# Optimization experiments

Measured on AMD Instinct MI355X. Metric: run time of the kernel, lower is better.

## Reference

```python
import jax, jax.numpy as jnp
import numpy as np

N = 10000          # nodes
E = 160000         # random edges (self-loops added in reference, as PyG does)
HEADS = 32
DIMS = [4, 128, 512, 1028]
NEG_SLOPE_ATT = 0.2    # GATv2Conv default negative_slope
NEG_SLOPE_ACT = 0.01   # torch.nn.LeakyReLU default


def setup_inputs() -> dict:
    key = jax.random.key(0)
    ks = jax.random.split(key, 32)
    inp = {}
    inp["x"] = jax.random.normal(ks[0], (N, DIMS[0]), dtype=jnp.float32)
    inp["edge_index"] = jax.random.randint(ks[1], (2, E), 0, N, dtype=jnp.int32)
    k = 2
    for l in range(3):
        fi, fo = DIMS[l], DIMS[l + 1]
        s_in = 1.0 / np.sqrt(fi)
        s_att = 1.0 / np.sqrt(fo)
        inp[f"W{l+1}l"] = (jax.random.normal(ks[k], (fi, HEADS * fo)) * s_in).astype(jnp.float32); k += 1
        inp[f"b{l+1}l"] = jnp.zeros((HEADS * fo,), jnp.float32)
        inp[f"W{l+1}r"] = (jax.random.normal(ks[k], (fi, HEADS * fo)) * s_in).astype(jnp.float32); k += 1
        inp[f"b{l+1}r"] = jnp.zeros((HEADS * fo,), jnp.float32)
        inp[f"att{l+1}"] = (jax.random.normal(ks[k], (HEADS, fo)) * s_att).astype(jnp.float32); k += 1
        inp[f"bias{l+1}"] = jnp.zeros((fo,), jnp.float32)
    return inp


def gatv2_layer(x, src, dst, Wl, bl, Wr, br, att, bias):
    # x: [N, fi]; src/dst: [E'] (self-loops included); att: [H, C]
    H, C = att.shape
    n = x.shape[0]
    xl = (x @ Wl + bl).reshape(n, H, C)  # source transform
    xr = (x @ Wr + br).reshape(n, H, C)  # target transform

    def per_head(args):
        xlh, xrh, ah = args  # [N,C], [N,C], [C]
        s = jax.nn.leaky_relu(xlh[src] + xrh[dst], NEG_SLOPE_ATT)  # [E',C]
        e = s @ ah  # [E'] attention logits
        m = jax.ops.segment_max(e, dst, num_segments=n)
        p = jnp.exp(e - m[dst])
        den = jax.ops.segment_sum(p, dst, num_segments=n)
        alpha = p / den[dst]  # edge-softmax per destination
        return jax.ops.segment_sum(alpha[:, None] * xlh[src], dst, num_segments=n)  # [N,C]

    # iterate heads sequentially to keep peak memory at O(E*C), not O(E*H*C)
    out = jax.lax.map(per_head, (jnp.moveaxis(xl, 1, 0), jnp.moveaxis(xr, 1, 0), att))  # [H,N,C]
    return out.mean(axis=0) + bias  # concat=False -> head mean


def reference(x, edge_index, W1l, b1l, W1r, b1r, att1, bias1,
              W2l, b2l, W2r, b2r, att2, bias2,
              W3l, b3l, W3r, b3r, att3, bias3):
    n = x.shape[0]
    loop = jnp.arange(n, dtype=edge_index.dtype)
    src = jnp.concatenate([edge_index[0], loop])
    dst = jnp.concatenate([edge_index[1], loop])
    h = gatv2_layer(x, src, dst, W1l, b1l, W1r, b1r, att1, bias1)
    h = jax.nn.leaky_relu(h, NEG_SLOPE_ACT)
    h = gatv2_layer(h, src, dst, W2l, b2l, W2r, b2r, att2, bias2)
    h = jax.nn.leaky_relu(h, NEG_SLOPE_ACT)
    h = gatv2_layer(h, src, dst, W3l, b3l, W3r, b3r, att3, bias3)
    return h
```

## Files before the change

kernel.cpp:

```cpp
#include <hip/hip_runtime.h>
#include <cstddef>
#include <cstdint>


#define HEADS 32
#define SLOPE_ATT 0.2f
#define SLOPE_ACT 0.01f

typedef __bf16 bf16_t;
typedef __bf16 bf16x8 __attribute__((ext_vector_type(8)));
typedef float f32x16 __attribute__((ext_vector_type(16)));

#define GLDS16(gp, lp)                                                        \
  __builtin_amdgcn_global_load_lds(                                           \
      (const __attribute__((address_space(1))) void*)(gp),                    \
      (__attribute__((address_space(3))) void*)(lp), 16, 0, 0)


__global__ __launch_bounds__(256) void init_counts_kernel(int* counts, int n) {
  int i = blockIdx.x * 256 + threadIdx.x;
  if (i < n) counts[i] = 1;
}

__global__ __launch_bounds__(256) void count_kernel(const int* __restrict__ dst, int* counts, int E) {
  int e = blockIdx.x * 256 + threadIdx.x;
  if (e < E) atomicAdd(&counts[dst[e]], 1);
}

__global__ __launch_bounds__(1024) void scan_kernel(const int* __restrict__ counts,
                                                    int* __restrict__ row_ptr,
                                                    int* __restrict__ cursor, int n) {
  __shared__ int sums[1024];
  int t = threadIdx.x;
// ... 40 lines not shown
                                                       bf16_t* __restrict__ hi,
                                                       bf16_t* __restrict__ lo,
                                                       int M, int Mpad, int K) {
  int t = blockIdx.x * 256 + threadIdx.x;
  int kchunks = K >> 3;
  int total = Mpad * kchunks;
  if (t >= total) return;
  int kc = t % kchunks;
  int m = t / kchunks;
  int mt = m >> 7, ml = m & 127;
  size_t o = ((size_t)(mt * kchunks + kc)) * 1024 + (size_t)ml * 8;
  float v[8];
  if (m < M) {
    float4 a = *(const float4*)(X + (size_t)m * K + kc * 8);
    float4 b = *(const float4*)(X + (size_t)m * K + kc * 8 + 4);
    v[0] = a.x; v[1] = a.y; v[2] = a.z; v[3] = a.w;
    v[4] = b.x; v[5] = b.y; v[6] = b.z; v[7] = b.w;
  } else {
#pragma unroll
    for (int i = 0; i < 8; i++) v[i] = 0.f;
  }
  union { bf16_t h[8]; float4 f; } uh, ul;
#pragma unroll
  for (int i = 0; i < 8; i++) {
    bf16_t h = (bf16_t)v[i];
    uh.h[i] = h;
    ul.h[i] = (bf16_t)(v[i] - (float)h);
  }
  *(float4*)(hi + o) = uh.f;
  *(float4*)(lo + o) = ul.f;
}


__global__ __launch_bounds__(256) void pack_w_group_kernel(const float* __restrict__ Wl,
                                                           const float* __restrict__ Wr,
                                                           bf16_t* __restrict__ hL, bf16_t* __restrict__ lL,
                                                           bf16_t* __restrict__ hR, bf16_t* __restrict__ lR,
                                                           int K, int C, int Npad, int ldW,
                                                           int h0, int G) {
  int side = blockIdx.y;
  const float* W = side ? Wr : Wl;
  bf16_t* Hi = side ? hR : hL;
  bf16_t* Lo = side ? lR : lL;
  int kchunks = K >> 3;
  int perhead = Npad * kchunks;
  int t = blockIdx.x * 256 + threadIdx.x;
  if (t >= G * perhead) return;
  int g = t / perhead, rem = t % perhead;
  int n = rem % Npad, kc = rem / Npad;
  int nt = n >> 7, nl = n & 127;
  size_t o = (size_t)g * Npad * K + ((size_t)(nt * kchunks + kc)) * 1024 + (size_t)nl * 8;
  int col0 = (h0 + g) * C;
  union { bf16_t hh[8]; float4 f; } uh, ul;
#pragma unroll
  for (int kk = 0; kk < 8; kk++) {
    int k = kc * 8 + kk;
    float v = (n < C) ? W[(size_t)k * ldW + col0 + n] : 0.f;
    bf16_t hv = (bf16_t)v;
    uh.hh[kk] = hv;
    ul.hh[kk] = (bf16_t)(v - (float)hv);
  }
  *(float4*)(Hi + o) = uh.f;
  *(float4*)(Lo + o) = ul.f;
}


__global__ __launch_bounds__(256) void gemm_mfma_v6(const bf16_t* __restrict__ Xh,
                                                    const bf16_t* __restrict__ Xl,
                                                    const bf16_t* __restrict__ BhL,
                                                    const bf16_t* __restrict__ BlL,
                                                    const bf16_t* __restrict__ BhR,
                                                    const bf16_t* __restrict__ BlR,
                                                    size_t bHeadStride,
                                                    const float* __restrict__ bl,
                                                    const float* __restrict__ br,
                                                    float* __restrict__ outL,
                                                    float* __restrict__ outR,
                                                    size_t outHeadStride,
                                                    int M, int K, int C, int h0) {
  int gx = gridDim.x, gy = gridDim.y, gz = gridDim.z;
  int nwg = gx * gy * gz;
  int p = blockIdx.x + gx * (blockIdx.y + gy * blockIdx.z);
  int q = nwg >> 3, r = nwg & 7;
  int xcd = p & 7, slot = p >> 3;
  int lid = (xcd < r ? xcd * (q + 1) : r * (q + 1) + (xcd - r) * q) + slot;
  const int NY = 8;
  int xzsz = gx * gz;
  int fullr = gy / NY;
  int lidf = fullr * NY * xzsz;
  int rectbase, ny, rem;
  if (lid < lidf) {
    int rect = lid / (NY * xzsz);
    rem = lid - rect * (NY * xzsz);
    rectbase = rect * NY;
    ny = NY;
  } else {
    rem = lid - lidf;
    rectbase = fullr * NY;
    ny = gy - rectbase;
  }
  int xz = rem / ny;
  int yl = rem - xz * ny;
  int bx = xz % gx;
  int bz = xz / gx;
  int by = rectbase + yl;

  int g = bz >> 1, side = bz & 1;
  const bf16_t* Bh = (side ? BhR : BhL) + (size_t)g * bHeadStride;
  const bf16_t* Bl = (side ? BlR : BlL) + (size_t)g * bHeadStride;
  const float* bias = side ? br : bl;
  float* out = (side ? outR : outL) + (size_t)g * outHeadStride;
  int col0 = (h0 + g) * C;

  __shared__ __align__(16) bf16_t AsH[4 * 128 * 8];
  __shared__ __align__(16) bf16_t AsL[4 * 128 * 8];
  __shared__ __align__(16) bf16_t BsH[4 * 128 * 8];
  __shared__ __align__(16) bf16_t BsL[4 * 128 * 8];

  int tid = threadIdx.x;
  int wave = tid >> 6, lane = tid & 63;
  int l31 = lane & 31, lhalf = lane >> 5;
  int mt = by;
  int ntb = bx * 128;
  int m0 = mt * 128;
  int kchunks = K >> 3;

  const bf16_t* Ah = Xh + (size_t)mt * K * 128;
  const bf16_t* Al = Xl + (size_t)mt * K * 128;
  const bf16_t* Bhp = Bh + (size_t)bx * kchunks * 1024;
  const bf16_t* Blp = Bl + (size_t)bx * kchunks * 1024;

  auto* asH3 = (__attribute__((address_space(3))) bf16_t*)AsH;
  auto* asL3 = (__attribute__((address_space(3))) bf16_t*)AsL;
  auto* bsH3 = (__attribute__((address_space(3))) bf16_t*)BsH;
  auto* bsL3 = (__attribute__((address_space(3))) bf16_t*)BsL;

  f32x16 acc[4];
#pragma unroll
  for (int i = 0; i < 4; i++)
#pragma unroll
    for (int rr = 0; rr < 16; rr++) acc[i][rr] = 0.f;

  for (int k0 = 0; k0 < K; k0 += 32) {
    int kc0 = k0 >> 3;
#pragma unroll
    for (int rr = 0; rr < 2; rr++) {
      int idx = tid + 256 * rr;
      size_t off = ((size_t)(kc0 + (idx >> 7))) * 1024 + (size_t)(idx & 127) * 8;
      int li = idx * 8;
      GLDS16(Ah + off, asH3 + li);
      GLDS16(Al + off, asL3 + li);
      GLDS16(Bhp + off, bsH3 + li);
      GLDS16(Blp + off, bsL3 + li);
    }
    __syncthreads();

#pragma unroll
    for (int s = 0; s < 2; s++) {
      int c = s * 2 + lhalf;
      int abase = (c * 128 + wave * 32 + l31) * 8;
      bf16x8 ah = *(const bf16x8*)&AsH[abase];
      bf16x8 al = *(const bf16x8*)&AsL[abase];
#pragma unroll
      for (int nt = 0; nt < 4; nt++) {
        int bbase = (c * 128 + nt * 32 + l31) * 8;
        bf16x8 bh = *(const bf16x8*)&BsH[bbase];
        bf16x8 blo = *(const bf16x8*)&BsL[bbase];
        acc[nt] = __builtin_amdgcn_mfma_f32_32x32x16_bf16(ah, bh, acc[nt], 0, 0, 0);
        acc[nt] = __builtin_amdgcn_mfma_f32_32x32x16_bf16(ah, blo, acc[nt], 0, 0, 0);
        acc[nt] = __builtin_amdgcn_mfma_f32_32x32x16_bf16(al, bh, acc[nt], 0, 0, 0);
      }
    }
    __syncthreads();
  }

#pragma unroll
  for (int nt = 0; nt < 4; nt++) {
    int n = ntb + nt * 32 + l31;
    if (n >= C) continue;
    float bv = bias[col0 + n];
#pragma unroll
    for (int rr = 0; rr < 16; rr++) {
      int row = (rr & 3) + 8 * (rr >> 2) + 4 * lhalf;
      int m = m0 + wave * 32 + row;
      if (m < M) out[(size_t)m * C + n] = acc[nt][rr] + bv;
    }
  }
}


#define BM 128
#define BN 128
#define BK 16
#define LDA (BM + 4)
#define LDB (BN + 4)

__global__ __launch_bounds__(256) void gemm128(const float* __restrict__ X,
                                               const float* __restrict__ Wl,
                                               const float* __restrict__ Wr,
                                               const float* __restrict__ bl,
                                               const float* __restrict__ br,
                                               float* __restrict__ outL,
                                               float* __restrict__ outR,
                                               int M, int K, int C, int ldW, int col0) {
  const float* W = blockIdx.z ? Wr : Wl;
  const float* bias = blockIdx.z ? br : bl;
  float* out = blockIdx.z ? outR : outL;

  __shared__ __align__(16) float As[BK][LDA];
  __shared__ __align__(16) float Bs[BK][LDB];

  int t = threadIdx.x;
  int tx = t & 15, ty = t >> 4;
  int m0 = blockIdx.y * BM, n0 = blockIdx.x * BN;

  float acc00[4][4] = {}, acc01[4][4] = {}, acc10[4][4] = {}, acc11[4][4] = {};

  for (int k0 = 0; k0 < K; k0 += BK) {
// ... 41 lines not shown
          acc00[i][j] += af0[i] * bf0[j];
          acc01[i][j] += af0[i] * bf1[j];
          acc10[i][j] += af1[i] * bf0[j];
          acc11[i][j] += af1[i] * bf1[j];
        }
    }
    __syncthreads();
  }

#pragma unroll
  for (int ma = 0; ma < 2; ma++) {
#pragma unroll
    for (int i = 0; i < 4; i++) {
      int m = m0 + ma * 64 + ty * 4 + i;
      if (m >= M) continue;
#pragma unroll
      for (int nb = 0; nb < 2; nb++) {
        int n = n0 + nb * 64 + tx * 4;
        float (*blk)[4] = (ma == 0) ? ((nb == 0) ? acc00 : acc01)
                                    : ((nb == 0) ? acc10 : acc11);
        if (n + 3 < C) {
          float4 bv = *(const float4*)(bias + col0 + n);
          float4 o = make_float4(blk[i][0] + bv.x, blk[i][1] + bv.y,
                                 blk[i][2] + bv.z, blk[i][3] + bv.w);
          *(float4*)(out + (size_t)m * C + n) = o;
        }
      }
    }
  }
}


template <int F4PT, int WIDTH>
__global__ __launch_bounds__(256) void edge_fused_multi(const int* __restrict__ row_ptr,
                                                        const int* __restrict__ col_src,
                                                        const float* __restrict__ xl,
                                                        const float* __restrict__ xr,
                                                        int ld4, size_t hstride4,
                                                        const float* __restrict__ att,
                                                        float* __restrict__ acc,
                                                        int C, int head0, int G) {
  constexpr int NG = 256 / WIDTH;
  constexpr int ROW = F4PT * WIDTH;
  constexpr int ITER = (ROW + 255) / 256;
  constexpr bool STASH = (F4PT >= 3);
  int node = blockIdx.x;
  int tid = threadIdx.x;
  int grp = tid / WIDTH, lane = tid % WIDTH;
  int C4 = C >> 2;
  int s = row_ptr[node], t = row_ptr[node + 1];

  __shared__ __align__(16) float4 slab[NG][ROW];
  __shared__ float mred[NG], dred[NG];

  float4 vtot[ITER];
#pragma unroll
  for (int it = 0; it < ITER; it++) vtot[it] = make_float4(0.f, 0.f, 0.f, 0.f);

  for (int g = 0; g < G; g++) {
    const float4* xlb = (const float4*)xl + (size_t)g * hstride4;
    const float4* xrp = (const float4*)xr + (size_t)g * hstride4 + (size_t)node * ld4;
    const float4* ap = (const float4*)(att + (size_t)g * C);

    float4 xr4[F4PT], a4[F4PT], o4[F4PT];
#pragma unroll
    for (int k = 0; k < F4PT; k++) {
      int c4 = k * WIDTH + lane;
      bool ok = (c4 < C4);
      xr4[k] = ok ? xrp[c4] : make_float4(0.f, 0.f, 0.f, 0.f);
      a4[k] = ok ? ap[c4] : make_float4(0.f, 0.f, 0.f, 0.f);
      o4[k] = make_float4(0.f, 0.f, 0.f, 0.f);
    }
    float m = -1e30f, den = 0.f;

    for (int j = s + grp; j < t; j += NG) {
      int src = col_src[j];
      const float4* xlp = xlb + (size_t)src * ld4;
      float4 x4[F4PT];
      float e = 0.f;
#pragma unroll
      for (int k = 0; k < F4PT; k++) {
        int c4 = k * WIDTH + lane;
        float4 xv = (c4 < C4) ? xlp[c4] : make_float4(0.f, 0.f, 0.f, 0.f);
        if constexpr (STASH) slab[grp][k * WIDTH + lane] = xv;
        else x4[k] = xv;
        float v;
        v = xv.x + xr4[k].x; v = fmaxf(v, SLOPE_ATT * v); e = fmaf(a4[k].x, v, e);
        v = xv.y + xr4[k].y; v = fmaxf(v, SLOPE_ATT * v); e = fmaf(a4[k].y, v, e);
        v = xv.z + xr4[k].z; v = fmaxf(v, SLOPE_ATT * v); e = fmaf(a4[k].z, v, e);
        v = xv.w + xr4[k].w; v = fmaxf(v, SLOPE_ATT * v); e = fmaf(a4[k].w, v, e);
      }
#pragma unroll
      for (int off = 1; off < WIDTH; off <<= 1) e += __shfl_xor(e, off, 64);

      if (e <= m) {
        float p = __expf(e - m);
        den += p;
#pragma unroll
        for (int k = 0; k < F4PT; k++) {
          float4 xv;
          if constexpr (STASH) xv = slab[grp][k * WIDTH + lane];
          else xv = x4[k];
          o4[k].x = fmaf(p, xv.x, o4[k].x); o4[k].y = fmaf(p, xv.y, o4[k].y);
          o4[k].z = fmaf(p, xv.z, o4[k].z); o4[k].w = fmaf(p, xv.w, o4[k].w);
        }
      } else {
        float sc = __expf(m - e);
        den = fmaf(den, sc, 1.f);
#pragma unroll
        for (int k = 0; k < F4PT; k++) {
          float4 xv;
          if constexpr (STASH) xv = slab[grp][k * WIDTH + lane];
          else xv = x4[k];
          o4[k].x = fmaf(o4[k].x, sc, xv.x); o4[k].y = fmaf(o4[k].y, sc, xv.y);
          o4[k].z = fmaf(o4[k].z, sc, xv.z); o4[k].w = fmaf(o4[k].w, sc, xv.w);
        }
        m = e;
      }
    }

    if (lane == 0) { mred[grp] = m; dred[grp] = den; }
    __syncthreads();
    float M2 = -1e30f;
#pragma unroll
    for (int i = 0; i < NG; i++) M2 = fmaxf(M2, mred[i]);
    float dtot = 0.f;
#pragma unroll
    for (int i = 0; i < NG; i++) dtot += dred[i] * __expf(mred[i] - M2);
    float f = __expf(m - M2);
#pragma unroll
    for (int k = 0; k < F4PT; k++) {
      float4 w4 = make_float4(o4[k].x * f, o4[k].y * f, o4[k].z * f, o4[k].w * f);
      slab[grp][k * WIDTH + lane] = w4;
    }
    __syncthreads();
    float inv = 1.0f / dtot;
#pragma unroll
    for (int it = 0; it < ITER; it++) {
      int c4 = tid + it * 256;
      if (c4 < ROW && c4 < C4) {
        float sx = 0.f, sy = 0.f, sz = 0.f, sw = 0.f;
#pragma unroll
        for (int i = 0; i < NG; i++) {
          float4 sv = slab[i][c4];
          sx += sv.x; sy += sv.y; sz += sv.z; sw += sv.w;
        }
        vtot[it].x = fmaf(sx, inv, vtot[it].x);
        vtot[it].y = fmaf(sy, inv, vtot[it].y);
        vtot[it].z = fmaf(sz, inv, vtot[it].z);
        vtot[it].w = fmaf(sw, inv, vtot[it].w);
      }
    }
    __syncthreads();
  }

  float4* accp = (float4*)(acc + (size_t)node * C);
#pragma unroll
  for (int it = 0; it < ITER; it++) {
    int c4 = tid + it * 256;
    if (c4 < ROW && c4 < C4) {
      if (head0 == 0) {
        accp[c4] = vtot[it];
      } else {
        float4 prev = accp[c4];
        accp[c4] = make_float4(prev.x + vtot[it].x, prev.y + vtot[it].y,
                               prev.z + vtot[it].z, prev.w + vtot[it].w);
      }
    }
  }
}


__global__ __launch_bounds__(256) void finalize_kernel(const float* __restrict__ acc,
                                                       const float* __restrict__ bias,
                                                       float* __restrict__ out,
                                                       int total, int C, int apply_act) {
  int i = blockIdx.x * 256 + threadIdx.x;
  if (i >= total) return;
  int c = i % C;
  float v = acc[i] * (1.0f / 32.0f) + bias[c];
  if (apply_act) v = fmaxf(v, SLOPE_ACT * v);
  out[i] = v;
}


static inline size_t align16(size_t x) { return (x + 15) & ~size_t(15); }

extern "C" void kernel_launch(void* const* d_in, const int* in_sizes, int n_in,
                              void* d_out, int out_size, void* d_ws, size_t ws_size,
                              hipStream_t stream) {
  const float* x0 = (const float*)d_in[0];
  const int* ei = (const int*)d_in[1];

  const int N = in_sizes[0] / 4;
  const int E = in_sizes[1] / 2;
  const int ETOT = E + N;
  const int MTILES = (N + 127) / 128;
  const int MPAD = MTILES * 128;

  struct LayerP { const float *Wl, *bl, *Wr, *br, *att, *bias; int fi, fo; };
  LayerP L[3] = {
      {(const float*)d_in[2],  (const float*)d_in[3],  (const float*)d_in[4],
       (const float*)d_in[5],  (const float*)d_in[6],  (const float*)d_in[7],  4, 128},
      {(const float*)d_in[8],  (const float*)d_in[9],  (const float*)d_in[10],
       (const float*)d_in[11], (const float*)d_in[12], (const float*)d_in[13], 128, 512},
      {(const float*)d_in[14], (const float*)d_in[15], (const float*)d_in[16],
       (const float*)d_in[17], (const float*)d_in[18], (const float*)d_in[19], 512, 1028},
  };

  char* w = (char*)d_ws;
  auto alloc = [&](size_t bytes) { char* p = w; w += align16(bytes); return p; };
  int* counts   = (int*)alloc((size_t)N * 4);
  int* row_ptr  = (int*)alloc((size_t)(N + 1) * 4);
  int* cursor   = (int*)alloc((size_t)N * 4);
  int* col_src  = (int*)alloc((size_t)ETOT * 4);
  int* col_dst  = (int*)alloc((size_t)ETOT * 4);
  float* xlh    = (float*)alloc((size_t)N * 2056 * 4);
  float* xrh    = (float*)alloc((size_t)N * 2056 * 4);
  float* h1     = (float*)alloc((size_t)N * 128 * 4);
  float* h2     = (float*)alloc((size_t)N * 512 * 4);
  float* acc12  = (float*)alloc((size_t)N * 512 * 4);
  bf16_t* xph   = (bf16_t*)alloc((size_t)MPAD * 512 * 2);
  bf16_t* xpl   = (bf16_t*)alloc((size_t)MPAD * 512 * 2);
  const size_t WPK3 = (size_t)2 * 1152 * 512;
  bf16_t* w3hL  = (bf16_t*)alloc(WPK3 * 2);
  bf16_t* w3lL  = (bf16_t*)alloc(WPK3 * 2);
  bf16_t* w3hR  = (bf16_t*)alloc(WPK3 * 2);
  bf16_t* w3lR  = (bf16_t*)alloc(WPK3 * 2);
  const size_t WPK2 = (size_t)HEADS * 512 * 128;
  bf16_t* w2hL  = (bf16_t*)alloc(WPK2 * 2);
  bf16_t* w2lL  = (bf16_t*)alloc(WPK2 * 2);
  bf16_t* w2hR  = (bf16_t*)alloc(WPK2 * 2);
  bf16_t* w2lR  = (bf16_t*)alloc(WPK2 * 2);

  init_counts_kernel<<<(N + 255) / 256, 256, 0, stream>>>(counts, N);
  count_kernel<<<(E + 255) / 256, 256, 0, stream>>>(ei + E, counts, E);
  scan_kernel<<<1, 1024, 0, stream>>>(counts, row_ptr, cursor, N);
  scatter_edges_kernel<<<(E + 255) / 256, 256, 0, stream>>>(ei, cursor, col_src, col_dst, E);
  scatter_loops_kernel<<<(N + 255) / 256, 256, 0, stream>>>(cursor, col_src, col_dst, N);

  {
    int C = 128;
    float* acc = acc12;
    for (int g = 0; g < 4; g++) {
      dim3 ggrid(8, MTILES, 2);
      gemm128<<<ggrid, 256, 0, stream>>>(x0, L[0].Wl, L[0].Wr, L[0].bl, L[0].br,
                                         xlh, xrh, N, 4, 1024, HEADS * C, g * 1024);
      edge_fused_multi<1, 32><<<N, 256, 0, stream>>>(row_ptr, col_src, xlh, xrh,
                                                     256, (size_t)32,
                                                     L[0].att + (size_t)(g * 8) * C,
                                                     acc, C, g * 8, 8);
    }
    finalize_kernel<<<((size_t)N * C + 255) / 256, 256, 0, stream>>>(acc, L[0].bias, h1,
                                                                     N * C, C, 1);
  }

  {
    int fi = 128, C = 512, ldW = HEADS * C, Npadh = 512, G = 4;
    float* acc = acc12;
    size_t NC = (size_t)N * C;
    int total = MPAD * (fi >> 3);
    cvt_pack_kernel<<<(total + 255) / 256, 256, 0, stream>>>(h1, xph, xpl, N, MPAD, fi);
    int wtotal = HEADS * Npadh * (fi >> 3);
    dim3 wgrid((wtotal + 255) / 256, 2);
    pack_w_group_kernel<<<wgrid, 256, 0, stream>>>(L[1].Wl, L[1].Wr, w2hL, w2lL, w2hR, w2lR,
                                                   fi, C, Npadh, ldW, 0, HEADS);
    size_t hstride = (size_t)Npadh * fi;
    for (int h0 = 0; h0 < HEADS; h0 += G) {
      dim3 ggrid(Npadh / 128, MTILES, 2 * G);
      gemm_mfma_v6<<<ggrid, 256, 0, stream>>>(xph, xpl,
                                              w2hL + h0 * hstride, w2lL + h0 * hstride,
                                              w2hR + h0 * hstride, w2lR + h0 * hstride,
                                              hstride, L[1].bl, L[1].br,
                                              xlh, xrh, NC, N, fi, C, h0);
      edge_fused_multi<2, 64><<<N, 256, 0, stream>>>(row_ptr, col_src, xlh, xrh,
                                                     C / 4, NC / 4,
                                                     L[1].att + (size_t)h0 * C,
                                                     acc, C, h0, G);
    }
    finalize_kernel<<<((size_t)N * C + 255) / 256, 256, 0, stream>>>(acc, L[1].bias, h2,
                                                                     N * C, C, 1);
  }

  {
    int fi = 512, C = 1028, ldW = HEADS * C, Npadh = 1152, G = 2;
    float* acc = (float*)d_out;
    size_t NC = (size_t)N * C;
    int total = MPAD * (fi >> 3);
    cvt_pack_kernel<<<(total + 255) / 256, 256, 0, stream>>>(h2, xph, xpl, N, MPAD, fi);
    size_t hstride = (size_t)Npadh * fi;
    for (int h0 = 0; h0 < HEADS; h0 += G) {
      int wtotal = G * Npadh * (fi >> 3);
      dim3 wgrid((wtotal + 255) / 256, 2);
      pack_w_group_kernel<<<wgrid, 256, 0, stream>>>(L[2].Wl, L[2].Wr, w3hL, w3lL, w3hR, w3lR,
                                                     fi, C, Npadh, ldW, h0, G);
      dim3 ggrid(Npadh / 128, MTILES, 2 * G);
      gemm_mfma_v6<<<ggrid, 256, 0, stream>>>(xph, xpl, w3hL, w3lL, w3hR, w3lR,
                                              hstride, L[2].bl, L[2].br,
                                              xlh, xrh, NC, N, fi, C, h0);
      edge_fused_multi<5, 64><<<N, 256, 0, stream>>>(row_ptr, col_src, xlh, xrh,
                                                     C / 4, NC / 4,
                                                     L[2].att + (size_t)h0 * C,
                                                     acc, C, h0, G);
    }
    finalize_kernel<<<((size_t)N * C + 255) / 256, 256, 0, stream>>>(acc, L[2].bias, (float*)d_out,
                                                                     N * C, C, 0);
  }
}
```

Baseline: 9.145 ms.

## Overlap next head-group GEMM and weight pack with current edge kernel in one launch

Merges the edge-attention pass for head group g, the MFMA GEMM for group g+1 and the weight packing for group g+2 into one persistent-style launch, with blocks dispatched by block index and the xl/xr and packed-weight buffers double-buffered. This hides the GEMM and pack work behind the memory-bound edge pass and cuts the number of launches and serialization points. Layers 2 and 3 move to smaller head groups (G=4 to 2, and 2 to 1) so the two stages can pipeline. The cost is that shared memory is sized for the larger of the two roles, which may lower occupancy, and the ordering between stages relies on consecutive launches in the same stream.

```diff
diff --git a/kernel.cpp b/kernel.cpp
--- a/kernel.cpp
+++ b/kernel.cpp
@@ -105,19 +105,21 @@
 }
 
 
-__global__ __launch_bounds__(256) void pack_w_group_kernel(const float* __restrict__ Wl,
-                                                           const float* __restrict__ Wr,
-                                                           bf16_t* __restrict__ hL, bf16_t* __restrict__ lL,
-                                                           bf16_t* __restrict__ hR, bf16_t* __restrict__ lR,
-                                                           int K, int C, int Npad, int ldW,
-                                                           int h0, int G) {
-  int side = blockIdx.y;
+__device__ __forceinline__ void pack_body(int pb, int perSide,
+                                          const float* __restrict__ Wl,
+                                          const float* __restrict__ Wr,
+                                          bf16_t* __restrict__ hL, bf16_t* __restrict__ lL,
+                                          bf16_t* __restrict__ hR, bf16_t* __restrict__ lR,
+                                          int K, int C, int Npad, int ldW,
+                                          int h0, int G) {
+  int side = pb / perSide;
+  int px = pb % perSide;
   const float* W = side ? Wr : Wl;
   bf16_t* Hi = side ? hR : hL;
   bf16_t* Lo = side ? lR : lL;
   int kchunks = K >> 3;
   int perhead = Npad * kchunks;
-  int t = blockIdx.x * 256 + threadIdx.x;
+  int t = px * 256 + threadIdx.x;
   if (t >= G * perhead) return;
   int g = t / perhead, rem = t % perhead;
   int n = rem % Npad, kc = rem / Npad;
@@ -137,23 +139,33 @@
   *(float4*)(Lo + o) = ul.f;
 }
 
-
-__global__ __launch_bounds__(256) void gemm_mfma_v6(const bf16_t* __restrict__ Xh,
-                                                    const bf16_t* __restrict__ Xl,
-                                                    const bf16_t* __restrict__ BhL,
-                                                    const bf16_t* __restrict__ BlL,
-                                                    const bf16_t* __restrict__ BhR,
-                                                    const bf16_t* __restrict__ BlR,
-                                                    size_t bHeadStride,
-                                                    const float* __restrict__ bl,
-                                                    const float* __restrict__ br,
-                                                    float* __restrict__ outL,
-                                                    float* __restrict__ outR,
-                                                    size_t outHeadStride,
-                                                    int M, int K, int C, int h0) {
-  int gx = gridDim.x, gy = gridDim.y, gz = gridDim.z;
+__global__ __launch_bounds__(256) void pack_w_group_kernel(const float* __restrict__ Wl,
+                                                           const float* __restrict__ Wr,
+                                                           bf16_t* hL, bf16_t* lL,
+                                                           bf16_t* hR, bf16_t* lR,
+                                                           int K, int C, int Npad, int ldW,
+                                                           int h0, int G) {
+  pack_body(blockIdx.y * gridDim.x + blockIdx.x, gridDim.x,
+            Wl, Wr, hL, lL, hR, lR, K, C, Npad, ldW, h0, G);
+}
+
+
+__device__ __forceinline__ void gemm_body(int p, int gx, int gy, int gz,
+                                          const bf16_t* __restrict__ Xh,
+                                          const bf16_t* __restrict__ Xl,
+                                          const bf16_t* __restrict__ BhL,
+                                          const bf16_t* __restrict__ BlL,
+                                          const bf16_t* __restrict__ BhR,
+                                          const bf16_t* __restrict__ BlR,
+                                          size_t bHeadStride,
+                                          const float* __restrict__ bl,
+                                          const float* __restrict__ br,
+                                          float* __restrict__ outL,
+                                          float* __restrict__ outR,
+                                          size_t outHeadStride,
+                                          int M, int K, int C, int h0,
+                                          char* smem) {
   int nwg = gx * gy * gz;
-  int p = blockIdx.x + gx * (blockIdx.y + gy * blockIdx.z);
   int q = nwg >> 3, r = nwg & 7;
   int xcd = p & 7, slot = p >> 3;
   int lid = (xcd < r ? xcd * (q + 1) : r * (q + 1) + (xcd - r) * q) + slot;
@@ -185,10 +197,10 @@
   float* out = (side ? outR : outL) + (size_t)g * outHeadStride;
   int col0 = (h0 + g) * C;
 
-  __shared__ __align__(16) bf16_t AsH[4 * 128 * 8];
-  __shared__ __align__(16) bf16_t AsL[4 * 128 * 8];
-  __shared__ __align__(16) bf16_t BsH[4 * 128 * 8];
-  __shared__ __align__(16) bf16_t BsL[4 * 128 * 8];
+  bf16_t* AsH = (bf16_t*)smem;
+  bf16_t* AsL = (bf16_t*)(smem + 8192);
+  bf16_t* BsH = (bf16_t*)(smem + 16384);
+  bf16_t* BsL = (bf16_t*)(smem + 24576);
 
   int tid = threadIdx.x;
   int wave = tid >> 6, lane = tid & 63;
@@ -232,13 +244,13 @@
     for (int s = 0; s < 2; s++) {
       int c = s * 2 + lhalf;
       int abase = (c * 128 + wave * 32 + l31) * 8;
-      bf16x8 ah = *(const bf16x8*)&AsH[abase];
-      bf16x8 al = *(const bf16x8*)&AsL[abase];
+      bf16x8 ah = *(const bf16x8*)(AsH + abase);
+      bf16x8 al = *(const bf16x8*)(AsL + abase);
 #pragma unroll
       for (int nt = 0; nt < 4; nt++) {
         int bbase = (c * 128 + nt * 32 + l31) * 8;
-        bf16x8 bh = *(const bf16x8*)&BsH[bbase];
-        bf16x8 blo = *(const bf16x8*)&BsL[bbase];
+        bf16x8 bh = *(const bf16x8*)(BsH + bbase);
+        bf16x8 blo = *(const bf16x8*)(BsL + bbase);
         acc[nt] = __builtin_amdgcn_mfma_f32_32x32x16_bf16(ah, bh, acc[nt], 0, 0, 0);
         acc[nt] = __builtin_amdgcn_mfma_f32_32x32x16_bf16(ah, blo, acc[nt], 0, 0, 0);
         acc[nt] = __builtin_amdgcn_mfma_f32_32x32x16_bf16(al, bh, acc[nt], 0, 0, 0);
@@ -364,26 +376,26 @@
 
 
 template <int F4PT, int WIDTH>
-__global__ __launch_bounds__(256) void edge_fused_multi(const int* __restrict__ row_ptr,
-                                                        const int* __restrict__ col_src,
-                                                        const float* __restrict__ xl,
-                                                        const float* __restrict__ xr,
-                                                        int ld4, size_t hstride4,
-                                                        const float* __restrict__ att,
-                                                        float* __restrict__ acc,
-                                                        int C, int head0, int G) {
+__device__ __forceinline__ void edge_body(const int* __restrict__ row_ptr,
+                                          const int* __restrict__ col_src,
+                                          const float* __restrict__ xl,
+                                          const float* __restrict__ xr,
+                                          int ld4, size_t hstride4,
+                                          const float* __restrict__ att,
+                                          float* __restrict__ acc,
+                                          int C, int head0, int G, int node,
+                                          char* smem) {
   constexpr int NG = 256 / WIDTH;
   constexpr int ROW = F4PT * WIDTH;
   constexpr int ITER = (ROW + 255) / 256;
   constexpr bool STASH = (F4PT >= 3);
-  int node = blockIdx.x;
+  float4 (*slab)[ROW] = (float4 (*)[ROW])smem;
+  float* mred = (float*)(smem + (size_t)NG * ROW * 16);
+  float* dred = mred + NG;
   int tid = threadIdx.x;
   int grp = tid / WIDTH, lane = tid % WIDTH;
   int C4 = C >> 2;
   int s = row_ptr[node], t = row_ptr[node + 1];
-
-  __shared__ __align__(16) float4 slab[NG][ROW];
-  __shared__ float mred[NG], dred[NG];
 
   float4 vtot[ITER];
 #pragma unroll
@@ -499,6 +511,67 @@
                                prev.z + vtot[it].z, prev.w + vtot[it].w);
       }
     }
+  }
+}
+
+
+template <int F4PT, int WIDTH>
+__global__ __launch_bounds__(256) void edge_solo(const int* __restrict__ row_ptr,
+                                                 const int* __restrict__ col_src,
+                                                 const float* __restrict__ xl,
+                                                 const float* __restrict__ xr,
+                                                 int ld4, size_t hstride4,
+                                                 const float* __restrict__ att,
+                                                 float* __restrict__ acc,
+                                                 int C, int head0, int G) {
+  constexpr int NG = 256 / WIDTH;
+  constexpr int ROW = F4PT * WIDTH;
+  __shared__ __align__(16) char smem[NG * ROW * 16 + 2 * NG * 4];
+  edge_body<F4PT, WIDTH>(row_ptr, col_src, xl, xr, ld4, hstride4, att, acc,
+                         C, head0, G, blockIdx.x, smem);
+}
+
+
+template <int F4PT, int WIDTH>
+__global__ __launch_bounds__(256) void fused_step(
+    const int* __restrict__ row_ptr, const int* __restrict__ col_src,
+    const float* __restrict__ exl, const float* __restrict__ exr,
+    int eld4, size_t ehstride4, const float* __restrict__ eatt,
+    float* __restrict__ eacc, int Ce, int ehead0, int Ge, int nEdge,
+    int gx, int gy, int gz,
+    const bf16_t* __restrict__ Xh, const bf16_t* __restrict__ Xl,
+    const bf16_t* __restrict__ BhL, const bf16_t* __restrict__ BlL,
+    const bf16_t* __restrict__ BhR, const bf16_t* __restrict__ BlR,
+    size_t bHeadStride, const float* __restrict__ gbl, const float* __restrict__ gbr,
+    float* __restrict__ outL, float* __restrict__ outR, size_t outHeadStride,
+    int M, int K, int Cg, int h0g,
+    int packPerSide, const float* __restrict__ pWl, const float* __restrict__ pWr,
+    bf16_t* __restrict__ phL, bf16_t* __restrict__ plL,
+    bf16_t* __restrict__ phR, bf16_t* __restrict__ plR,
+    int pK, int pC, int pNpad, int pldW, int ph0, int pG) {
+  constexpr int NG = 256 / WIDTH;
+  constexpr int ROW = F4PT * WIDTH;
+  constexpr int EDGE_BYTES = NG * ROW * 16 + 2 * NG * 4;
+  constexpr int LDS_SZ = (EDGE_BYTES > 32768) ? EDGE_BYTES : 32768;
+  __shared__ __align__(16) char smem[LDS_SZ];
+
+  int fb = blockIdx.x;
+  if (fb < nEdge) {
+    edge_body<F4PT, WIDTH>(row_ptr, col_src, exl, exr, eld4, ehstride4, eatt,
+                           eacc, Ce, ehead0, Ge, fb, smem);
+    return;
+  }
+  fb -= nEdge;
+  int nwg = gx * gy * gz;
+  if (fb < nwg) {
+    gemm_body(fb, gx, gy, gz, Xh, Xl, BhL, BlL, BhR, BlR, bHeadStride,
+              gbl, gbr, outL, outR, outHeadStride, M, K, Cg, h0g, smem);
+    return;
+  }
+  fb -= nwg;
+  if (packPerSide > 0 && fb < 2 * packPerSide) {
+    pack_body(fb, packPerSide, pWl, pWr, phL, plL, phR, plR,
+              pK, pC, pNpad, pldW, ph0, pG);
   }
 }
 
@@ -554,11 +627,11 @@
   float* acc12  = (float*)alloc((size_t)N * 512 * 4);
   bf16_t* xph   = (bf16_t*)alloc((size_t)MPAD * 512 * 2);
   bf16_t* xpl   = (bf16_t*)alloc((size_t)MPAD * 512 * 2);
-  const size_t WPK3 = (size_t)2 * 1152 * 512;
-  bf16_t* w3hL  = (bf16_t*)alloc(WPK3 * 2);
-  bf16_t* w3lL  = (bf16_t*)alloc(WPK3 * 2);
-  bf16_t* w3hR  = (bf16_t*)alloc(WPK3 * 2);
-  bf16_t* w3lR  = (bf16_t*)alloc(WPK3 * 2);
+  const size_t W3G = (size_t)1152 * 512;
+  bf16_t* w3hL  = (bf16_t*)alloc(2 * W3G * 2);
+  bf16_t* w3lL  = (bf16_t*)alloc(2 * W3G * 2);
+  bf16_t* w3hR  = (bf16_t*)alloc(2 * W3G * 2);
+  bf16_t* w3lR  = (bf16_t*)alloc(2 * W3G * 2);
   const size_t WPK2 = (size_t)HEADS * 512 * 128;
   bf16_t* w2hL  = (bf16_t*)alloc(WPK2 * 2);
   bf16_t* w2lL  = (bf16_t*)alloc(WPK2 * 2);
@@ -578,62 +651,95 @@
       dim3 ggrid(8, MTILES, 2);
       gemm128<<<ggrid, 256, 0, stream>>>(x0, L[0].Wl, L[0].Wr, L[0].bl, L[0].br,
                                          xlh, xrh, N, 4, 1024, HEADS * C, g * 1024);
-      edge_fused_multi<1, 32><<<N, 256, 0, stream>>>(row_ptr, col_src, xlh, xrh,
-                                                     256, (size_t)32,
-                                                     L[0].att + (size_t)(g * 8) * C,
-                                                     acc, C, g * 8, 8);
+      edge_solo<1, 32><<<N, 256, 0, stream>>>(row_ptr, col_src, xlh, xrh,
+                                              256, (size_t)32,
+                                              L[0].att + (size_t)(g * 8) * C,
+                                              acc, C, g * 8, 8);
     }
     finalize_kernel<<<((size_t)N * C + 255) / 256, 256, 0, stream>>>(acc, L[0].bias, h1,
                                                                      N * C, C, 1);
   }
 
   {
-    int fi = 128, C = 512, ldW = HEADS * C, Npadh = 512, G = 4;
+    int fi = 128, C = 512, ldW = HEADS * C, Npadh = 512, G = 2;
     float* acc = acc12;
-    size_t NC = (size_t)N * C;
+    size_t bufStride = (size_t)N * 1024;
+    size_t hstr = (size_t)N * C;
     int total = MPAD * (fi >> 3);
     cvt_pack_kernel<<<(total + 255) / 256, 256, 0, stream>>>(h1, xph, xpl, N, MPAD, fi);
     int wtotal = HEADS * Npadh * (fi >> 3);
     dim3 wgrid((wtotal + 255) / 256, 2);
     pack_w_group_kernel<<<wgrid, 256, 0, stream>>>(L[1].Wl, L[1].Wr, w2hL, w2lL, w2hR, w2lR,
                                                    fi, C, Npadh, ldW, 0, HEADS);
-    size_t hstride = (size_t)Npadh * fi;
-    for (int h0 = 0; h0 < HEADS; h0 += G) {
-      dim3 ggrid(Npadh / 128, MTILES, 2 * G);
-      gemm_mfma_v6<<<ggrid, 256, 0, stream>>>(xph, xpl,
-                                              w2hL + h0 * hstride, w2lL + h0 * hstride,
-                                              w2hR + h0 * hstride, w2lR + h0 * hstride,
-                                              hstride, L[1].bl, L[1].br,
-                                              xlh, xrh, NC, N, fi, C, h0);
-      edge_fused_multi<2, 64><<<N, 256, 0, stream>>>(row_ptr, col_src, xlh, xrh,
-                                                     C / 4, NC / 4,
-                                                     L[1].att + (size_t)h0 * C,
-                                                     acc, C, h0, G);
+    size_t whstride = (size_t)Npadh * fi;
+    int gx = Npadh / 128, gy = MTILES, gz = 2 * G;
+    int nwg = gx * gy * gz;
+    const int NGR = HEADS / G;
+    fused_step<2, 64><<<nwg, 256, 0, stream>>>(
+        row_ptr, col_src, xlh, xrh, C / 4, hstr / 4, L[1].att, acc, C, 0, G, 0,
+        gx, gy, gz, xph, xpl, w2hL, w2lL, w2hR, w2lR, whstride,
+        L[1].bl, L[1].br, xlh, xrh, hstr, N, fi, C, 0,
+        0, L[1].Wl, L[1].Wr, w2hL, w2lL, w2hR, w2lR, fi, C, Npadh, ldW, 0, 0);
+    for (int g = 0; g < NGR; g++) {
+      int gn = g + 1;
+      bool hasG = gn < NGR;
+      int gni = hasG ? gn : 0;
+      int tot = N + (hasG ? nwg : 0);
+      fused_step<2, 64><<<tot, 256, 0, stream>>>(
+          row_ptr, col_src,
+          xlh + (size_t)(g & 1) * bufStride, xrh + (size_t)(g & 1) * bufStride,
+          C / 4, hstr / 4, L[1].att + (size_t)(G * g) * C, acc, C, G * g, G, N,
+          hasG ? gx : 0, gy, gz, xph, xpl,
+          w2hL + (size_t)(G * gni) * whstride, w2lL + (size_t)(G * gni) * whstride,
+          w2hR + (size_t)(G * gni) * whstride, w2lR + (size_t)(G * gni) * whstride,
+          whstride, L[1].bl, L[1].br,
+          xlh + (size_t)(gni & 1) * bufStride, xrh + (size_t)(gni & 1) * bufStride,
+          hstr, N, fi, C, G * gni,
+          0, L[1].Wl, L[1].Wr, w2hL, w2lL, w2hR, w2lR, fi, C, Npadh, ldW, 0, 0);
     }
     finalize_kernel<<<((size_t)N * C + 255) / 256, 256, 0, stream>>>(acc, L[1].bias, h2,
                                                                      N * C, C, 1);
   }
 
   {
-    int fi = 512, C = 1028, ldW = HEADS * C, Npadh = 1152, G = 2;
+    int fi = 512, C = 1028, ldW = HEADS * C, Npadh = 1152, G = 1;
     float* acc = (float*)d_out;
-    size_t NC = (size_t)N * C;
+    size_t bufStride = (size_t)N * 1028;
     int total = MPAD * (fi >> 3);
     cvt_pack_kernel<<<(total + 255) / 256, 256, 0, stream>>>(h2, xph, xpl, N, MPAD, fi);
-    size_t hstride = (size_t)Npadh * fi;
-    for (int h0 = 0; h0 < HEADS; h0 += G) {
-      int wtotal = G * Npadh * (fi >> 3);
-      dim3 wgrid((wtotal + 255) / 256, 2);
-      pack_w_group_kernel<<<wgrid, 256, 0, stream>>>(L[2].Wl, L[2].Wr, w3hL, w3lL, w3hR, w3lR,
-                                                     fi, C, Npadh, ldW, h0, G);
-      dim3 ggrid(Npadh / 128, MTILES, 2 * G);
-      gemm_mfma_v6<<<ggrid, 256, 0, stream>>>(xph, xpl, w3hL, w3lL, w3hR, w3lR,
-                                              hstride, L[2].bl, L[2].br,
-                                              xlh, xrh, NC, N, fi, C, h0);
-      edge_fused_multi<5, 64><<<N, 256, 0, stream>>>(row_ptr, col_src, xlh, xrh,
-                                                     C / 4, NC / 4,
-                                                     L[2].att + (size_t)h0 * C,
-                                                     acc, C, h0, G);
+    int gx = Npadh / 128, gy = MTILES, gz = 2;
+    int nwg = gx * gy * gz;
+    int pwtotal = Npadh * (fi >> 3);
+    int pps = (pwtotal + 255) / 256;
+    dim3 wgrid(pps, 2);
+    pack_w_group_kernel<<<wgrid, 256, 0, stream>>>(L[2].Wl, L[2].Wr,
+                                                   w3hL, w3lL, w3hR, w3lR,
+                                                   fi, C, Npadh, ldW, 0, 1);
+    fused_step<5, 64><<<nwg + 2 * pps, 256, 0, stream>>>(
+        row_ptr, col_src, xlh, xrh, C / 4, 0, L[2].att, acc, C, 0, G, 0,
+        gx, gy, gz, xph, xpl, w3hL, w3lL, w3hR, w3lR, W3G,
+        L[2].bl, L[2].br, xlh, xrh, bufStride, N, fi, C, 0,
+        pps, L[2].Wl, L[2].Wr, w3hL + W3G, w3lL + W3G, w3hR + W3G, w3lR + W3G,
+        fi, C, Npadh, ldW, 1, 1);
+    for (int g = 0; g < HEADS; g++) {
+      int gn = g + 1, gp = g + 2;
+      bool hasG = gn < HEADS, hasP = gp < HEADS;
+      int gni = hasG ? gn : 0, gpi = hasP ? gp : 0;
+      int tot = N + (hasG ? nwg : 0) + (hasP ? 2 * pps : 0);
+      fused_step<5, 64><<<tot, 256, 0, stream>>>(
+          row_ptr, col_src,
+          xlh + (size_t)(g & 1) * bufStride, xrh + (size_t)(g & 1) * bufStride,
+          C / 4, 0, L[2].att + (size_t)g * C, acc, C, g, 1, N,
+          hasG ? gx : 0, gy, gz, xph, xpl,
+          w3hL + (size_t)(gni & 1) * W3G, w3lL + (size_t)(gni & 1) * W3G,
+          w3hR + (size_t)(gni & 1) * W3G, w3lR + (size_t)(gni & 1) * W3G,
+          W3G, L[2].bl, L[2].br,
+          xlh + (size_t)(gni & 1) * bufStride, xrh + (size_t)(gni & 1) * bufStride,
+          bufStride, N, fi, C, gni,
+          hasP ? pps : 0, L[2].Wl, L[2].Wr,
+          w3hL + (size_t)(gpi & 1) * W3G, w3lL + (size_t)(gpi & 1) * W3G,
+          w3hR + (size_t)(gpi & 1) * W3G, w3lR + (size_t)(gpi & 1) * W3G,
+          fi, C, Npadh, ldW, gpi, 1);
     }
     finalize_kernel<<<((size_t)N * C + 255) / 256, 256, 0, stream>>>(acc, L[2].bias, (float*)d_out,
                                                                      N * C, C, 0);
```

New measurement: 11.58 ms. +26.6%, slower.

## Store source-side projections as fp16 to halve edge gather traffic

Applied to the files above, without the earlier changes.

The MFMA GEMM epilogue now writes the source-side (xl) projection for layers 2 and 3 as fp16 with a padded row stride, while xr stays fp32. A new edge kernel, edge_fused_half, gathers the fp16 rows with 16-byte loads, converts them to float and runs the same online-softmax aggregation. The aim is to halve the bytes fetched per edge in the gather, which dominates the edge phase. The cost is reduced precision in the attention logits and in the aggregated values, which could move the output past the tolerance.

```diff
diff --git a/kernel.cpp b/kernel.cpp
--- a/kernel.cpp
+++ b/kernel.cpp
@@ -1,4 +1,5 @@
 #include <hip/hip_runtime.h>
+#include <hip/hip_fp16.h>
 #include <cstddef>
 #include <cstdint>
 
@@ -147,9 +148,10 @@
                                                     size_t bHeadStride,
                                                     const float* __restrict__ bl,
                                                     const float* __restrict__ br,
-                                                    float* __restrict__ outL,
+                                                    __half* __restrict__ outLh,
+                                                    size_t outLStrideH, int ldh,
                                                     float* __restrict__ outR,
-                                                    size_t outHeadStride,
+                                                    size_t outRStride,
                                                     int M, int K, int C, int h0) {
   int gx = gridDim.x, gy = gridDim.y, gz = gridDim.z;
   int nwg = gx * gy * gz;
@@ -182,7 +184,6 @@
   const bf16_t* Bh = (side ? BhR : BhL) + (size_t)g * bHeadStride;
   const bf16_t* Bl = (side ? BlR : BlL) + (size_t)g * bHeadStride;
   const float* bias = side ? br : bl;
-  float* out = (side ? outR : outL) + (size_t)g * outHeadStride;
   int col0 = (h0 + g) * C;
 
   __shared__ __align__(16) bf16_t AsH[4 * 128 * 8];
@@ -247,16 +248,36 @@
     __syncthreads();
   }
 
-#pragma unroll
-  for (int nt = 0; nt < 4; nt++) {
-    int n = ntb + nt * 32 + l31;
-    if (n >= C) continue;
-    float bv = bias[col0 + n];
-#pragma unroll
-    for (int rr = 0; rr < 16; rr++) {
-      int row = (rr & 3) + 8 * (rr >> 2) + 4 * lhalf;
-      int m = m0 + wave * 32 + row;
-      if (m < M) out[(size_t)m * C + n] = acc[nt][rr] + bv;
+  if (side == 0) {
+    __half* out = outLh + (size_t)g * outLStrideH;
+#pragma unroll
+    for (int nt = 0; nt < 4; nt++) {
+      int n = ntb + nt * 32 + l31;
+      if (n >= ldh) continue;
+      float bv = (n < C) ? bias[col0 + n] : 0.f;
+#pragma unroll
+      for (int rr = 0; rr < 16; rr++) {
+        int row = (rr & 3) + 8 * (rr >> 2) + 4 * lhalf;
+        int m = m0 + wave * 32 + row;
+        if (m < M) {
+          float val = (n < C) ? (acc[nt][rr] + bv) : 0.f;
+          out[(size_t)m * ldh + n] = __float2half(val);
+        }
+      }
+    }
+  } else {
+    float* out = outR + (size_t)g * outRStride;
+#pragma unroll
+    for (int nt = 0; nt < 4; nt++) {
+      int n = ntb + nt * 32 + l31;
+      if (n >= C) continue;
+      float bv = bias[col0 + n];
+#pragma unroll
+      for (int rr = 0; rr < 16; rr++) {
+        int row = (rr & 3) + 8 * (rr >> 2) + 4 * lhalf;
+        int m = m0 + wave * 32 + row;
+        if (m < M) out[(size_t)m * C + n] = acc[nt][rr] + bv;
+      }
     }
   }
 }
@@ -375,7 +396,6 @@
   constexpr int NG = 256 / WIDTH;
   constexpr int ROW = F4PT * WIDTH;
   constexpr int ITER = (ROW + 255) / 256;
-  constexpr bool STASH = (F4PT >= 3);
   int node = blockIdx.x;
   int tid = threadIdx.x;
   int grp = tid / WIDTH, lane = tid % WIDTH;
@@ -413,14 +433,12 @@
 #pragma unroll
       for (int k = 0; k < F4PT; k++) {
         int c4 = k * WIDTH + lane;
-        float4 xv = (c4 < C4) ? xlp[c4] : make_float4(0.f, 0.f, 0.f, 0.f);
-        if constexpr (STASH) slab[grp][k * WIDTH + lane] = xv;
-        else x4[k] = xv;
+        x4[k] = (c4 < C4) ? xlp[c4] : make_float4(0.f, 0.f, 0.f, 0.f);
         float v;
-        v = xv.x + xr4[k].x; v = fmaxf(v, SLOPE_ATT * v); e = fmaf(a4[k].x, v, e);
-        v = xv.y + xr4[k].y; v = fmaxf(v, SLOPE_ATT * v); e = fmaf(a4[k].y, v, e);
-        v = xv.z + xr4[k].z; v = fmaxf(v, SLOPE_ATT * v); e = fmaf(a4[k].z, v, e);
-        v = xv.w + xr4[k].w; v = fmaxf(v, SLOPE_ATT * v); e = fmaf(a4[k].w, v, e);
+        v = x4[k].x + xr4[k].x; v = fmaxf(v, SLOPE_ATT * v); e = fmaf(a4[k].x, v, e);
+        v = x4[k].y + xr4[k].y; v = fmaxf(v, SLOPE_ATT * v); e = fmaf(a4[k].y, v, e);
+        v = x4[k].z + xr4[k].z; v = fmaxf(v, SLOPE_ATT * v); e = fmaf(a4[k].z, v, e);
+        v = x4[k].w + xr4[k].w; v = fmaxf(v, SLOPE_ATT * v); e = fmaf(a4[k].w, v, e);
       }
 #pragma unroll
       for (int off = 1; off < WIDTH; off <<= 1) e += __shfl_xor(e, off, 64);
@@ -430,22 +448,16 @@
         den += p;
 #pragma unroll
         for (int k = 0; k < F4PT; k++) {
-          float4 xv;
-          if constexpr (STASH) xv = slab[grp][k * WIDTH + lane];
-          else xv = x4[k];
-          o4[k].x = fmaf(p, xv.x, o4[k].x); o4[k].y = fmaf(p, xv.y, o4[k].y);
-          o4[k].z = fmaf(p, xv.z, o4[k].z); o4[k].w = fmaf(p, xv.w, o4[k].w);
+          o4[k].x = fmaf(p, x4[k].x, o4[k].x); o4[k].y = fmaf(p, x4[k].y, o4[k].y);
+          o4[k].z = fmaf(p, x4[k].z, o4[k].z); o4[k].w = fmaf(p, x4[k].w, o4[k].w);
         }
       } else {
         float sc = __expf(m - e);
         den = fmaf(den, sc, 1.f);
 #pragma unroll
         for (int k = 0; k < F4PT; k++) {
-          float4 xv;
-          if constexpr (STASH) xv = slab[grp][k * WIDTH + lane];
-          else xv = x4[k];
-          o4[k].x = fmaf(o4[k].x, sc, xv.x); o4[k].y = fmaf(o4[k].y, sc, xv.y);
-          o4[k].z = fmaf(o4[k].z, sc, xv.z); o4[k].w = fmaf(o4[k].w, sc, xv.w);
+          o4[k].x = fmaf(o4[k].x, sc, x4[k].x); o4[k].y = fmaf(o4[k].y, sc, x4[k].y);
+          o4[k].z = fmaf(o4[k].z, sc, x4[k].z); o4[k].w = fmaf(o4[k].w, sc, x4[k].w);
         }
         m = e;
       }
@@ -464,6 +476,183 @@
     for (int k = 0; k < F4PT; k++) {
       float4 w4 = make_float4(o4[k].x * f, o4[k].y * f, o4[k].z * f, o4[k].w * f);
       slab[grp][k * WIDTH + lane] = w4;
+    }
+    __syncthreads();
+    float inv = 1.0f / dtot;
+#pragma unroll
+    for (int it = 0; it < ITER; it++) {
+      int c4 = tid + it * 256;
+      if (c4 < ROW && c4 < C4) {
+        float sx = 0.f, sy = 0.f, sz = 0.f, sw = 0.f;
+#pragma unroll
+        for (int i = 0; i < NG; i++) {
+          float4 sv = slab[i][c4];
+          sx += sv.x; sy += sv.y; sz += sv.z; sw += sv.w;
+        }
+        vtot[it].x = fmaf(sx, inv, vtot[it].x);
+        vtot[it].y = fmaf(sy, inv, vtot[it].y);
+        vtot[it].z = fmaf(sz, inv, vtot[it].z);
+        vtot[it].w = fmaf(sw, inv, vtot[it].w);
+      }
+    }
+    __syncthreads();
+  }
+
+  float4* accp = (float4*)(acc + (size_t)node * C);
+#pragma unroll
+  for (int it = 0; it < ITER; it++) {
+    int c4 = tid + it * 256;
+    if (c4 < ROW && c4 < C4) {
+      if (head0 == 0) {
+        accp[c4] = vtot[it];
+      } else {
+        float4 prev = accp[c4];
+        accp[c4] = make_float4(prev.x + vtot[it].x, prev.y + vtot[it].y,
+                               prev.z + vtot[it].z, prev.w + vtot[it].w);
+      }
+    }
+  }
+}
+
+
+template <int HPT>
+__global__ __launch_bounds__(256) void edge_fused_half(const int* __restrict__ row_ptr,
+                                                       const int* __restrict__ col_src,
+                                                       const __half* __restrict__ xl,
+                                                       const float* __restrict__ xr,
+                                                       int ldh, size_t hstrH,
+                                                       int ldr4, size_t hstrR4,
+                                                       const float* __restrict__ att,
+                                                       float* __restrict__ acc,
+                                                       int C, int head0, int G) {
+  constexpr int NG = 4;
+  constexpr int ROW = 2 * HPT * 64;
+  constexpr int ITER = (ROW + 255) / 256;
+  constexpr bool STASH = (HPT >= 2);
+  int node = blockIdx.x;
+  int tid = threadIdx.x;
+  int grp = tid >> 6, lane = tid & 63;
+  int C4 = C >> 2;
+  int units = ldh >> 3;
+  int s = row_ptr[node], t = row_ptr[node + 1];
+
+  __shared__ __align__(16) float4 slab[NG][ROW];
+  __shared__ float mred[NG], dred[NG];
+
+  float4 vtot[ITER];
+#pragma unroll
+  for (int it = 0; it < ITER; it++) vtot[it] = make_float4(0.f, 0.f, 0.f, 0.f);
+
+  for (int g = 0; g < G; g++) {
+    const __half* xlb = xl + (size_t)g * hstrH;
+    const float4* xrp = (const float4*)xr + (size_t)g * hstrR4 + (size_t)node * ldr4;
+    const float4* ap = (const float4*)(att + (size_t)g * C);
+
+    float4 xr4[2 * HPT], a4[2 * HPT], o4[2 * HPT];
+#pragma unroll
+    for (int u = 0; u < HPT; u++) {
+      int unit = u * 64 + lane;
+#pragma unroll
+      for (int h = 0; h < 2; h++) {
+        int c4 = unit * 2 + h;
+        bool ok = (c4 < C4);
+        xr4[2 * u + h] = ok ? xrp[c4] : make_float4(0.f, 0.f, 0.f, 0.f);
+        a4[2 * u + h] = ok ? ap[c4] : make_float4(0.f, 0.f, 0.f, 0.f);
+        o4[2 * u + h] = make_float4(0.f, 0.f, 0.f, 0.f);
+      }
+    }
+    float m = -1e30f, den = 0.f;
+
+    for (int j = s + grp; j < t; j += NG) {
+      int src = col_src[j];
+      const __half* xrow = xlb + (size_t)src * ldh;
+      float4 x4[2 * HPT];
+      float e = 0.f;
+#pragma unroll
+      for (int u = 0; u < HPT; u++) {
+        int unit = u * 64 + lane;
+        uint4 raw = make_uint4(0u, 0u, 0u, 0u);
+        if (unit < units) raw = *(const uint4*)(xrow + (size_t)unit * 8);
+        union { uint4 q; __half2 h2[4]; } cv; cv.q = raw;
+        float2 p0 = __half22float2(cv.h2[0]);
+        float2 p1 = __half22float2(cv.h2[1]);
+        float2 p2 = __half22float2(cv.h2[2]);
+        float2 p3 = __half22float2(cv.h2[3]);
+        float4 f0 = make_float4(p0.x, p0.y, p1.x, p1.y);
+        float4 f1 = make_float4(p2.x, p2.y, p3.x, p3.y);
+        if constexpr (STASH) {
+          slab[grp][unit * 2 + 0] = f0;
+          slab[grp][unit * 2 + 1] = f1;
+        } else {
+          x4[2 * u] = f0; x4[2 * u + 1] = f1;
+        }
+        float v;
+        v = f0.x + xr4[2 * u].x; v = fmaxf(v, SLOPE_ATT * v); e = fmaf(a4[2 * u].x, v, e);
+        v = f0.y + xr4[2 * u].y; v = fmaxf(v, SLOPE_ATT * v); e = fmaf(a4[2 * u].y, v, e);
+        v = f0.z + xr4[2 * u].z; v = fmaxf(v, SLOPE_ATT * v); e = fmaf(a4[2 * u].z, v, e);
+        v = f0.w + xr4[2 * u].w; v = fmaxf(v, SLOPE_ATT * v); e = fmaf(a4[2 * u].w, v, e);
+        v = f1.x + xr4[2 * u + 1].x; v = fmaxf(v, SLOPE_ATT * v); e = fmaf(a4[2 * u + 1].x, v, e);
+        v = f1.y + xr4[2 * u + 1].y; v = fmaxf(v, SLOPE_ATT * v); e = fmaf(a4[2 * u + 1].y, v, e);
+        v = f1.z + xr4[2 * u + 1].z; v = fmaxf(v, SLOPE_ATT * v); e = fmaf(a4[2 * u + 1].z, v, e);
+        v = f1.w + xr4[2 * u + 1].w; v = fmaxf(v, SLOPE_ATT * v); e = fmaf(a4[2 * u + 1].w, v, e);
+      }
+#pragma unroll
+      for (int off = 1; off < 64; off <<= 1) e += __shfl_xor(e, off, 64);
+
+      if (e <= m) {
+        float p = __expf(e - m);
+        den += p;
+#pragma unroll
+        for (int u = 0; u < HPT; u++) {
+          int unit = u * 64 + lane;
+#pragma unroll
+          for (int h = 0; h < 2; h++) {
+            float4 xv;
+            if constexpr (STASH) xv = slab[grp][unit * 2 + h];
+            else xv = x4[2 * u + h];
+            int k = 2 * u + h;
+            o4[k].x = fmaf(p, xv.x, o4[k].x); o4[k].y = fmaf(p, xv.y, o4[k].y);
+            o4[k].z = fmaf(p, xv.z, o4[k].z); o4[k].w = fmaf(p, xv.w, o4[k].w);
+          }
+        }
+      } else {
+        float sc = __expf(m - e);
+        den = fmaf(den, sc, 1.f);
+#pragma unroll
+        for (int u = 0; u < HPT; u++) {
+          int unit = u * 64 + lane;
+#pragma unroll
+          for (int h = 0; h < 2; h++) {
+            float4 xv;
+            if constexpr (STASH) xv = slab[grp][unit * 2 + h];
+            else xv = x4[2 * u + h];
+            int k = 2 * u + h;
+            o4[k].x = fmaf(o4[k].x, sc, xv.x); o4[k].y = fmaf(o4[k].y, sc, xv.y);
+            o4[k].z = fmaf(o4[k].z, sc, xv.z); o4[k].w = fmaf(o4[k].w, sc, xv.w);
+          }
+        }
+        m = e;
+      }
+    }
+
+    if (lane == 0) { mred[grp] = m; dred[grp] = den; }
+    __syncthreads();
+    float M2 = -1e30f;
+#pragma unroll
+    for (int i = 0; i < NG; i++) M2 = fmaxf(M2, mred[i]);
+    float dtot = 0.f;
+#pragma unroll
+    for (int i = 0; i < NG; i++) dtot += dred[i] * __expf(mred[i] - M2);
+    float f = __expf(m - M2);
+#pragma unroll
+    for (int u = 0; u < HPT; u++) {
+      int unit = u * 64 + lane;
+#pragma unroll
+      for (int h = 0; h < 2; h++) {
+        int k = 2 * u + h;
+        slab[grp][unit * 2 + h] =
+            make_float4(o4[k].x * f, o4[k].y * f, o4[k].z * f, o4[k].w * f);
+      }
     }
     __syncthreads();
     float inv = 1.0f / dtot;
@@ -588,9 +777,8 @@
   }
 
   {
-    int fi = 128, C = 512, ldW = HEADS * C, Npadh = 512, G = 4;
+    int fi = 128, C = 512, ldW = HEADS * C, Npadh = 512, G = 4, ldh = 512;
     float* acc = acc12;
-    size_t NC = (size_t)N * C;
     int total = MPAD * (fi >> 3);
     cvt_pack_kernel<<<(total + 255) / 256, 256, 0, stream>>>(h1, xph, xpl, N, MPAD, fi);
     int wtotal = HEADS * Npadh * (fi >> 3);
@@ -598,29 +786,34 @@
     pack_w_group_kernel<<<wgrid, 256, 0, stream>>>(L[1].Wl, L[1].Wr, w2hL, w2lL, w2hR, w2lR,
                                                    fi, C, Npadh, ldW, 0, HEADS);
     size_t hstride = (size_t)Npadh * fi;
+    size_t strH = (size_t)N * ldh;
+    size_t strR = (size_t)N * C;
     for (int h0 = 0; h0 < HEADS; h0 += G) {
       dim3 ggrid(Npadh / 128, MTILES, 2 * G);
       gemm_mfma_v6<<<ggrid, 256, 0, stream>>>(xph, xpl,
                                               w2hL + h0 * hstride, w2lL + h0 * hstride,
                                               w2hR + h0 * hstride, w2lR + h0 * hstride,
                                               hstride, L[1].bl, L[1].br,
-                                              xlh, xrh, NC, N, fi, C, h0);
-      edge_fused_multi<2, 64><<<N, 256, 0, stream>>>(row_ptr, col_src, xlh, xrh,
-                                                     C / 4, NC / 4,
-                                                     L[1].att + (size_t)h0 * C,
-                                                     acc, C, h0, G);
+                                              (__half*)xlh, strH, ldh, xrh, strR,
+                                              N, fi, C, h0);
+      edge_fused_half<1><<<N, 256, 0, stream>>>(row_ptr, col_src,
+                                                (const __half*)xlh, xrh,
+                                                ldh, strH, C / 4, strR / 4,
+                                                L[1].att + (size_t)h0 * C,
+                                                acc, C, h0, G);
     }
     finalize_kernel<<<((size_t)N * C + 255) / 256, 256, 0, stream>>>(acc, L[1].bias, h2,
                                                                      N * C, C, 1);
   }
 
   {
-    int fi = 512, C = 1028, ldW = HEADS * C, Npadh = 1152, G = 2;
+    int fi = 512, C = 1028, ldW = HEADS * C, Npadh = 1152, G = 2, ldh = 1032;
     float* acc = (float*)d_out;
-    size_t NC = (size_t)N * C;
     int total = MPAD * (fi >> 3);
     cvt_pack_kernel<<<(total + 255) / 256, 256, 0, stream>>>(h2, xph, xpl, N, MPAD, fi);
     size_t hstride = (size_t)Npadh * fi;
+    size_t strH = (size_t)N * ldh;
+    size_t strR = (size_t)N * C;
     for (int h0 = 0; h0 < HEADS; h0 += G) {
       int wtotal = G * Npadh * (fi >> 3);
       dim3 wgrid((wtotal + 255) / 256, 2);
@@ -629,11 +822,13 @@
       dim3 ggrid(Npadh / 128, MTILES, 2 * G);
       gemm_mfma_v6<<<ggrid, 256, 0, stream>>>(xph, xpl, w3hL, w3lL, w3hR, w3lR,
                                               hstride, L[2].bl, L[2].br,
-                                              xlh, xrh, NC, N, fi, C, h0);
-      edge_fused_multi<5, 64><<<N, 256, 0, stream>>>(row_ptr, col_src, xlh, xrh,
-                                                     C / 4, NC / 4,
-                                                     L[2].att + (size_t)h0 * C,
-                                                     acc, C, h0, G);
+                                              (__half*)xlh, strH, ldh, xrh, strR,
+                                              N, fi, C, h0);
+      edge_fused_half<3><<<N, 256, 0, stream>>>(row_ptr, col_src,
+                                                (const __half*)xlh, xrh,
+                                                ldh, strH, C / 4, strR / 4,
+                                                L[2].att + (size_t)h0 * C,
+                                                acc, C, h0, G);
     }
     finalize_kernel<<<((size_t)N * C + 255) / 256, 256, 0, stream>>>(acc, L[2].bias, (float*)d_out,
                                                                      N * C, C, 0);
```

Result: faster. 8.771 ms (-4.1%).
